# Performance work log

Measured on AMD Instinct MI355X. Metric: run time of the kernel, lower is better.

The kernel has to match this reference:

```python
import jax, jax.numpy as jnp
import numpy as np

B, C, H, W = 4, 3, 256, 256
NCC = 64            # num_conv_channels
N_HIDDEN = 20 - 2   # hidden_block applied num_hiddel_blocks-2 times (shared weights)
EPS = 1e-5          # BatchNorm eps (eval mode: running stats; Dropout2d is identity in eval)


def _bayer_mask():
    # RGGB Bayer pattern: each channel sampled only at its sites, zeros elsewhere
    m = np.zeros((3, H, W), dtype=np.float32)
    m[0, 0::2, 0::2] = 1.0  # R
    m[1, 0::2, 1::2] = 1.0  # G
    m[1, 1::2, 0::2] = 1.0  # G
    m[2, 1::2, 1::2] = 1.0  # B
    return jnp.asarray(m)


def setup_inputs() -> dict:
    key = jax.random.key(0)
    ks = jax.random.split(key, 8)
    X = jax.random.uniform(ks[0], (B, C, H, W), dtype=jnp.float32) * _bayer_mask()[None]
    w_in = jax.random.normal(ks[1], (NCC, 3, 3, 3), dtype=jnp.float32) * 0.15
    b_in = jnp.zeros((NCC,), jnp.float32)
    w_h = jax.random.normal(ks[2], (NCC, NCC, 3, 3), dtype=jnp.float32) * 0.04
    b_h = jnp.zeros((NCC,), jnp.float32)
    w_out = jax.random.normal(ks[3], (3, NCC, 3, 3), dtype=jnp.float32) * 0.04
    b_out = jnp.zeros((3,), jnp.float32)
    def bn_params(n):
        return (jnp.ones((n,), jnp.float32), jnp.zeros((n,), jnp.float32),
                jnp.zeros((n,), jnp.float32), jnp.ones((n,), jnp.float32))
    g_in, be_in, m_in, v_in = bn_params(NCC)
    g_h, be_h, m_h, v_h = bn_params(NCC)
    g_out, be_out, m_out, v_out = bn_params(3)
    return dict(X=X, w_in=w_in, b_in=b_in, g_in=g_in, be_in=be_in, m_in=m_in, v_in=v_in,
                w_h=w_h, b_h=b_h, g_h=g_h, be_h=be_h, m_h=m_h, v_h=v_h,
                w_out=w_out, b_out=b_out, g_out=g_out, be_out=be_out, m_out=m_out, v_out=v_out)


def _conv(x, w, b):
    y = jax.lax.conv_general_dilated(x, w, (1, 1), ((1, 1), (1, 1)),
                                     dimension_numbers=('NCHW', 'OIHW', 'NCHW'))
    return y + b[None, :, None, None]


def _bn(x, g, be, m, v):
    scale = (g / jnp.sqrt(v + EPS))[None, :, None, None]
    return (x - m[None, :, None, None]) * scale + be[None, :, None, None]


def _interpolate_zeros(x):
    # Vectorized masked cross-neighbor average at zero sites, dividing by the
    # count of strictly-positive neighbors (zero-padded borders).
    p = jnp.pad(x, ((0, 0), (0, 0), (1, 1), (1, 1)))
    left = p[:, :, 1:-1, :-2]
    right = p[:, :, 1:-1, 2:]
    top = p[:, :, :-2, 1:-1]
    bottom = p[:, :, 2:, 1:-1]
    nb_sum = left + right + top + bottom
    nb_cnt = ((left > 0).astype(x.dtype) + (right > 0).astype(x.dtype)
              + (top > 0).astype(x.dtype) + (bottom > 0).astype(x.dtype))
    mean = jnp.where(nb_cnt > 0, nb_sum / jnp.maximum(nb_cnt, 1.0), 0.0)
    return jnp.where(x == 0, mean, x)


def reference(X, w_in, b_in, g_in, be_in, m_in, v_in,
              w_h, b_h, g_h, be_h, m_h, v_h,
              w_out, b_out, g_out, be_out, m_out, v_out):
    y = jax.nn.selu(_bn(_conv(X, w_in, b_in), g_in, be_in, m_in, v_in))

    def hidden(y, _):
        y = jax.nn.selu(_bn(_conv(y, w_h, b_h), g_h, be_h, m_h, v_h))
        return y, None

    y, _ = jax.lax.scan(hidden, y, None, length=N_HIDDEN)
    y = jax.nn.selu(_bn(_conv(y, w_out, b_out), g_out, be_out, m_out, v_out))
    return y + _interpolate_zeros(X)
```

## Files before the change

kernel.cpp:

```cpp
#include <hip/hip_runtime.h>

#define EPS 1e-5f
#define SELU_L 1.0507009873554805f
#define SELU_A 1.6732632423543772f
#define SELU_LA (SELU_L * SELU_A)

typedef _Float16 half8 __attribute__((ext_vector_type(8)));
typedef _Float16 half4 __attribute__((ext_vector_type(4)));
typedef float floatx4 __attribute__((ext_vector_type(4)));

__device__ __forceinline__ float selu_f(float x) {
    return x > 0.f ? SELU_L * x : SELU_LA * (__expf(x) - 1.f);
}

__device__ __forceinline__ void gload_lds16(const _Float16* g, _Float16* l) {
    __builtin_amdgcn_global_load_lds(
        (const __attribute__((address_space(1))) void*)g,
        (__attribute__((address_space(3))) void*)l, 16, 0, 0);
}

__global__ __launch_bounds__(256) void k_prep(
    const float* __restrict__ w_h, const float* __restrict__ w_in,
    const float* __restrict__ w_out, _Float16* __restrict__ wb_h,
    _Float16* __restrict__ wb_in, _Float16* __restrict__ wb_out,
    _Float16* __restrict__ zp)
{
    int i = blockIdx.x * 256 + threadIdx.x;
    if (i < 256) zp[i] = (_Float16)0.f;
    if (i < 36864) {
        int t = i >> 11;
        int rem = i & 2047;
        int mi = rem >> 9;
        int L = (rem >> 3) & 63;
        int j = i & 7;
        int co = mi * 16 + (L & 15);
        int ci = ((t & 1) << 5) + ((L >> 4) << 3) + j;
        int s = t >> 1;
        wb_h[i] = (_Float16)w_h[(co * 64 + ci) * 9 + s];
    } else if (i < 36864 + 2048) {
        int e = i - 36864;
        int mi = e >> 9;
        int L = (e >> 3) & 63;
        int j = e & 7;
        int co = mi * 16 + (L & 15);
        int k = ((L >> 4) << 3) + j;
        _Float16 val = (_Float16)0.f;
        if (k < 27) {
            int s = k / 3, ci = k - s * 3;
            val = (_Float16)w_in[(co * 3 + ci) * 9 + s];
        }
        wb_in[e] = val;
    } else if (i < 36864 + 2048 + 9216) {
        int e = i - 36864 - 2048;
        int t = e >> 9;
        int L = (e >> 3) & 63;
        int j = e & 7;
        int co = L & 15;
        int ci = ((t & 1) << 5) + ((L >> 4) << 3) + j;
        int s = t >> 1;
        _Float16 val = (_Float16)0.f;
        if (co < 3) val = (_Float16)w_out[(co * 64 + ci) * 9 + s];
        wb_out[e] = val;
    }
}

__global__ __launch_bounds__(256) void k_conv_in_mfma(
    const float* __restrict__ X, const _Float16* __restrict__ wb,
    const float* __restrict__ bconv, const float* __restrict__ g,
    const float* __restrict__ be, const float* __restrict__ bm,
    const float* __restrict__ bv, _Float16* __restrict__ dst)
{
    __shared__ float s_x[3][18][18];
    __shared__ float s_sc[64], s_bs[64];
    const int tid = threadIdx.x;
    const int w0 = blockIdx.x * 16, h0 = blockIdx.y * 16, b = blockIdx.z;

    if (tid < 64) {
        float sc = g[tid] * rsqrtf(bv[tid] + EPS);
        s_sc[tid] = sc;
        s_bs[tid] = (bconv[tid] - bm[tid]) * sc + be[tid];
    }
    for (int idx = tid; idx < 3 * 324; idx += 256) {
        int ci = idx / 324, rem = idx - ci * 324;
        int r = rem / 18, c = rem - r * 18;
        int gh = h0 - 1 + r, gw = w0 - 1 + c;
        float val = 0.f;
        if ((unsigned)gh < 256u && (unsigned)gw < 256u)
            val = X[((b * 3 + ci) << 16) + (gh << 8) + gw];
        s_x[ci][r][c] = val;
    }
    __syncthreads();

    const int wv = tid >> 6, L = tid & 63, quad = L >> 4, l15 = L & 15;
    half8 a[4];
    #pragma unroll
    for (int mi = 0; mi < 4; ++mi)
        a[mi] = *(const half8*)(wb + (mi * 64 + L) * 8);

    floatx4 acc[4][4];
    #pragma unroll
    for (int mi = 0; mi < 4; ++mi)
        #pragma unroll
        for (int ni = 0; ni < 4; ++ni) acc[mi][ni] = (floatx4){0.f, 0.f, 0.f, 0.f};

    #pragma unroll
    for (int ni = 0; ni < 4; ++ni) {
        half8 bfr;
        #pragma unroll
        for (int j = 0; j < 8; ++j) {
            int k = quad * 8 + j;
            float xv = 0.f;
            if (k < 27) {
                int s = k / 3, ci = k - s * 3;
                int kh = s / 3, kw = s - kh * 3;
                xv = s_x[ci][wv * 4 + ni + kh][l15 + kw];
            }
            bfr[j] = (_Float16)xv;
        }
        #pragma unroll
        for (int mi = 0; mi < 4; ++mi)
            acc[mi][ni] = __builtin_amdgcn_mfma_f32_16x16x32_f16(a[mi], bfr, acc[mi][ni], 0, 0, 0);
    }

    _Float16* db = dst + ((size_t)b << 22);
    #pragma unroll
    for (int mi = 0; mi < 4; ++mi) {
        const int cob = mi * 16 + quad * 4;
        floatx4 sc = *(const floatx4*)(&s_sc[cob]);
        floatx4 bs = *(const floatx4*)(&s_bs[cob]);
        #pragma unroll
        for (int ni = 0; ni < 4; ++ni) {
            half4 ov;
            #pragma unroll
            for (int r = 0; r < 4; ++r)
                ov[r] = (_Float16)selu_f(acc[mi][ni][r] * sc[r] + bs[r]);
            const int row = h0 + wv * 4 + ni, col = w0 + l15;
            *(half4*)(db + ((((row << 8) + col) << 6) + cob)) = ov;
        }
    }
}

__global__ __launch_bounds__(1024) void k_hidden_v13(
    const _Float16* __restrict__ src, const _Float16* __restrict__ wb,
    const float* __restrict__ bconv, const float* __restrict__ g,
    const float* __restrict__ be, const float* __restrict__ bm,
    const float* __restrict__ bv, const _Float16* __restrict__ zp,
    _Float16* __restrict__ dst)
{
    __shared__ _Float16 s_w[36864];
    __shared__ _Float16 s_act[2][20992];
    __shared__ float s_sc[64], s_bs[64];
    const int tid = threadIdx.x;
    const int wv = tid >> 6, L = tid & 63, quad = L >> 4, l15 = L & 15;
    const int rq = wv >> 2, mq = wv & 3;

    if (tid < 64) {
        float sc = g[tid] * rsqrtf(bv[tid] + EPS);
        s_sc[tid] = sc;
        s_bs[tid] = (bconv[tid] - bm[tid]) * sc + be[tid];
    }

    #pragma unroll
    for (int k = 0; k < 5; ++k) {
        const int wc = k * 16 + wv;
        if (wc < 72)
            gload_lds16(wb + ((wc << 6) + L) * 8, &s_w[wc << 9]);
    }

    auto stage = [&](int tau, int buf) {
        const int b = tau >> 8, rem = tau & 255;
        const int h0 = (rem >> 4) << 4, w0 = (rem & 15) << 4;
        const _Float16* sb = src + ((size_t)b << 22);
        #pragma unroll
        for (int k = 0; k < 3; ++k) {
            const int wc = k * 16 + wv;
            if (wc < 41) {
                const int p = (wc << 3) + (L >> 3);
                const int sd = (L & 7) ^ (p & 7);
                const int rp = p / 18, cl = p - rp * 18;
                const int gh = h0 - 1 + rp, gw = w0 - 1 + cl;
                const _Float16* gp = (p < 324 && (unsigned)gh < 256u && (unsigned)gw < 256u)
                    ? sb + ((((gh << 8) + gw) << 6) + (sd << 3)) : zp;
                gload_lds16(gp, &s_act[buf][wc << 9]);
            }
        }
    };

    const int tau0 = blockIdx.x << 2;
    stage(tau0, 0);
    __syncthreads();

    for (int ti = 0; ti < 4; ++ti) {
        const int tau = tau0 + ti, cur = ti & 1;
        if (ti < 3) stage(tau + 1, cur ^ 1);

        floatx4 acc[4];
        #pragma unroll
        for (int ni = 0; ni < 4; ++ni) acc[ni] = (floatx4){0.f, 0.f, 0.f, 0.f};

        const _Float16* bufp = &s_act[cur][0];
        #pragma unroll
        for (int h = 0; h < 2; ++h) {
            const int sb8 = (h << 2) + quad;
            #pragma unroll
            for (int kw = 0; kw < 3; ++kw) {
                half8 ac[3];
                #pragma unroll
                for (int kh = 0; kh < 3; ++kh) {
                    const int t = ((kh * 3 + kw) << 1) + h;
                    ac[kh] = *(const half8*)(&s_w[((t * 4 + mq) * 64 + L) * 8]);
                }
                #pragma unroll
                for (int j = 0; j < 6; ++j) {
                    const int p = (rq * 4 + j) * 18 + l15 + kw;
                    half8 bfr = *(const half8*)(bufp + (p << 6) + (((p & 7) ^ sb8) << 3));
                    #pragma unroll
                    for (int kh = 0; kh < 3; ++kh) {
                        const int ni = j - kh;
                        if (ni >= 0 && ni < 4)
                            acc[ni] = __builtin_amdgcn_mfma_f32_16x16x32_f16(ac[kh], bfr, acc[ni], 0, 0, 0);
                    }
                }
            }
        }

        const int b = tau >> 8, rem = tau & 255;
        const int h0 = (rem >> 4) << 4, w0 = (rem & 15) << 4;
        _Float16* db = dst + ((size_t)b << 22);
        const int cob = mq * 16 + quad * 4;
        floatx4 sc = *(const floatx4*)(&s_sc[cob]);
        floatx4 bs = *(const floatx4*)(&s_bs[cob]);
        #pragma unroll
        for (int ni = 0; ni < 4; ++ni) {
            half4 ov;
            #pragma unroll
            for (int r = 0; r < 4; ++r)
                ov[r] = (_Float16)selu_f(acc[ni][r] * sc[r] + bs[r]);
            const int row = h0 + rq * 4 + ni, col = w0 + l15;
            *(half4*)(db + ((((row << 8) + col) << 6) + cob)) = ov;
        }
        __syncthreads();
    }
}

__global__ __launch_bounds__(256) void k_conv_out_mfma(
    const _Float16* __restrict__ src, const _Float16* __restrict__ wb,
    const float* __restrict__ bconv, const float* __restrict__ g,
    const float* __restrict__ be, const float* __restrict__ bm,
    const float* __restrict__ bv, const float* __restrict__ X,
    float* __restrict__ out)
{
    __shared__ _Float16 s_in[324 * 72];
    const int tid = threadIdx.x;
    const int w0 = blockIdx.x * 16, h0 = blockIdx.y * 16, b = blockIdx.z;
    const _Float16* sb = src + ((size_t)b << 22);

    for (int idx = tid; idx < 2592; idx += 256) {
        int r = idx / 144, cpos = idx - r * 144;
        int col = cpos >> 3, sub = cpos & 7;
        int gh = h0 - 1 + r, gw = w0 - 1 + col;
        half8 val = {0, 0, 0, 0, 0, 0, 0, 0};
        if ((unsigned)gh < 256u && (unsigned)gw < 256u)
            val = *(const half8*)(sb + ((((gh << 8) + gw) << 6) + (sub << 3)));
        *(half8*)(&s_in[(r * 18 + col) * 72 + (sub << 3)]) = val;
    }
    __syncthreads();

    const int wv = tid >> 6, L = tid & 63, quad = L >> 4, l15 = L & 15;
    floatx4 acc[4];
    #pragma unroll
    for (int ni = 0; ni < 4; ++ni) acc[ni] = (floatx4){0.f, 0.f, 0.f, 0.f};

    #pragma unroll
    for (int t = 0; t < 18; ++t) {
        const int s = t >> 1, ci0 = (t & 1) << 5;
        const int kh = s / 3, kw = s - kh * 3;
        half8 a = *(const half8*)(wb + (t * 64 + L) * 8);
        #pragma unroll
        for (int ni = 0; ni < 4; ++ni) {
            const int row = wv * 4 + ni + kh, col = l15 + kw;
            half8 bfr = *(const half8*)(&s_in[(row * 18 + col) * 72 + ci0 + quad * 8]);
            acc[ni] = __builtin_amdgcn_mfma_f32_16x16x32_f16(a, bfr, acc[ni], 0, 0, 0);
        }
    }

    if (quad == 0) {
        float sc[3], bs[3];
        #pragma unroll
        for (int co = 0; co < 3; ++co) {
            sc[co] = g[co] * rsqrtf(bv[co] + EPS);
            bs[co] = (bconv[co] - bm[co]) * sc[co] + be[co];
        }
        #pragma unroll
        for (int ni = 0; ni < 4; ++ni) {
            const int h = h0 + wv * 4 + ni, wc = w0 + l15;
            #pragma unroll
            for (int co = 0; co < 3; ++co) {
                float val = selu_f(acc[ni][co] * sc[co] + bs[co]);
                const float* Xc = X + ((size_t)(b * 3 + co) << 16);
                float x = Xc[(h << 8) + wc];
                float res;
                if (x == 0.f) {
                    float lft = (wc > 0)   ? Xc[(h << 8) + wc - 1] : 0.f;
                    float rgt = (wc < 255) ? Xc[(h << 8) + wc + 1] : 0.f;
                    float top = (h > 0)    ? Xc[((h - 1) << 8) + wc] : 0.f;
                    float bot = (h < 255)  ? Xc[((h + 1) << 8) + wc] : 0.f;
                    float sm = lft + rgt + top + bot;
                    int cnt = (lft > 0.f) + (rgt > 0.f) + (top > 0.f) + (bot > 0.f);
                    res = cnt > 0 ? sm / (float)cnt : 0.f;
                } else {
                    res = x;
                }
                out[((b * 3 + co) << 16) + (h << 8) + wc] = val + res;
            }
        }
    }
}

extern "C" void kernel_launch(void* const* d_in, const int* in_sizes, int n_in,
                              void* d_out, int out_size, void* d_ws, size_t ws_size,
                              hipStream_t stream) {
    (void)in_sizes; (void)n_in; (void)out_size; (void)ws_size;
    const float* X    = (const float*)d_in[0];
    const float* w_in = (const float*)d_in[1];
    const float* b_in = (const float*)d_in[2];
    const float* g_in = (const float*)d_in[3];
    const float* be_in= (const float*)d_in[4];
    const float* m_in = (const float*)d_in[5];
    const float* v_in = (const float*)d_in[6];
    const float* w_h  = (const float*)d_in[7];
    const float* b_h  = (const float*)d_in[8];
    const float* g_h  = (const float*)d_in[9];
    const float* be_h = (const float*)d_in[10];
    const float* m_h  = (const float*)d_in[11];
    const float* v_h  = (const float*)d_in[12];
    const float* w_o  = (const float*)d_in[13];
    const float* b_o  = (const float*)d_in[14];
    const float* g_o  = (const float*)d_in[15];
    const float* be_o = (const float*)d_in[16];
    const float* m_o  = (const float*)d_in[17];
    const float* v_o  = (const float*)d_in[18];
    float* out = (float*)d_out;

    _Float16* act0  = (_Float16*)d_ws;
    _Float16* act1  = act0 + ((size_t)1 << 24);
    _Float16* wb_h  = act1 + ((size_t)1 << 24);
    _Float16* wb_in = wb_h + 36864;
    _Float16* wb_out= wb_in + 2048;
    _Float16* zp    = wb_out + 9216;

    dim3 grid(16, 16, 4), block(256);
    k_prep<<<188, 256, 0, stream>>>(w_h, w_in, w_o, wb_h, wb_in, wb_out, zp);
    k_conv_in_mfma<<<grid, block, 0, stream>>>(X, wb_in, b_in, g_in, be_in, m_in, v_in, act0);
    _Float16* src = act0;
    _Float16* dst = act1;
    for (int i = 0; i < 18; ++i) {
        k_hidden_v13<<<256, 1024, 0, stream>>>(src, wb_h, b_h, g_h, be_h, m_h, v_h, zp, dst);
        _Float16* t = src; src = dst; dst = t;
    }
    k_conv_out_mfma<<<grid, block, 0, stream>>>(src, wb_out, b_o, g_o, be_o, m_o, v_o, X, out);
}
```

Baseline: 597.9 us.

## Fuse eighteen hidden-layer launches into one persistent kernel with grid barrier

Replaces the 18 per-layer launches of the hidden conv kernel with a single persistent kernel. It loops over layers, ping-pongs between the two activation buffers, and separates layers with a software grid barrier (an atomic counter zeroed in the prep kernel). This is meant to remove per-launch overhead and the repeated reload of the weights into LDS. In exchange it adds barrier spin latency, relies on all 256 blocks being co-resident, and relies on cross-XCD cache coherence of activations written by other blocks.

```diff
diff --git a/kernel.cpp b/kernel.cpp
--- a/kernel.cpp
+++ b/kernel.cpp
@@ -23,9 +23,10 @@
     const float* __restrict__ w_h, const float* __restrict__ w_in,
     const float* __restrict__ w_out, _Float16* __restrict__ wb_h,
     _Float16* __restrict__ wb_in, _Float16* __restrict__ wb_out,
-    _Float16* __restrict__ zp)
+    _Float16* __restrict__ zp, unsigned* __restrict__ bar)
 {
     int i = blockIdx.x * 256 + threadIdx.x;
+    if (i == 0) *bar = 0u;
     if (i < 256) zp[i] = (_Float16)0.f;
     if (i < 36864) {
         int t = i >> 11;
@@ -140,12 +141,13 @@
     }
 }
 
-__global__ __launch_bounds__(1024) void k_hidden_v13(
-    const _Float16* __restrict__ src, const _Float16* __restrict__ wb,
+__global__ __launch_bounds__(1024) void k_hidden_all(
+    _Float16* __restrict__ act0, _Float16* __restrict__ act1,
+    const _Float16* __restrict__ wb,
     const float* __restrict__ bconv, const float* __restrict__ g,
     const float* __restrict__ be, const float* __restrict__ bm,
     const float* __restrict__ bv, const _Float16* __restrict__ zp,
-    _Float16* __restrict__ dst)
+    unsigned* __restrict__ bar)
 {
     __shared__ _Float16 s_w[36864];
     __shared__ _Float16 s_act[2][20992];
@@ -167,10 +169,10 @@
             gload_lds16(wb + ((wc << 6) + L) * 8, &s_w[wc << 9]);
     }
 
-    auto stage = [&](int tau, int buf) {
+    auto stage = [&](const _Float16* sp, int tau, int buf) {
         const int b = tau >> 8, rem = tau & 255;
         const int h0 = (rem >> 4) << 4, w0 = (rem & 15) << 4;
-        const _Float16* sb = src + ((size_t)b << 22);
+        const _Float16* sb = sp + ((size_t)b << 22);
         #pragma unroll
         for (int k = 0; k < 3; ++k) {
             const int wc = k * 16 + wv;
@@ -187,59 +189,80 @@
     };
 
     const int tau0 = blockIdx.x << 2;
-    stage(tau0, 0);
+    _Float16* src = act0;
+    _Float16* dst = act1;
+
+    stage(src, tau0, 0);
     __syncthreads();
 
-    for (int ti = 0; ti < 4; ++ti) {
-        const int tau = tau0 + ti, cur = ti & 1;
-        if (ti < 3) stage(tau + 1, cur ^ 1);
-
-        floatx4 acc[4];
-        #pragma unroll
-        for (int ni = 0; ni < 4; ++ni) acc[ni] = (floatx4){0.f, 0.f, 0.f, 0.f};
-
-        const _Float16* bufp = &s_act[cur][0];
-        #pragma unroll
-        for (int h = 0; h < 2; ++h) {
-            const int sb8 = (h << 2) + quad;
-            #pragma unroll
-            for (int kw = 0; kw < 3; ++kw) {
-                half8 ac[3];
+    for (int layer = 0; layer < 18; ++layer) {
+        for (int ti = 0; ti < 4; ++ti) {
+            const int tau = tau0 + ti, cur = ti & 1;
+            if (ti < 3) stage(src, tau + 1, cur ^ 1);
+
+            floatx4 acc[4];
+            #pragma unroll
+            for (int ni = 0; ni < 4; ++ni) acc[ni] = (floatx4){0.f, 0.f, 0.f, 0.f};
+
+            const _Float16* bufp = &s_act[cur][0];
+            #pragma unroll
+            for (int h = 0; h < 2; ++h) {
+                const int sb8 = (h << 2) + quad;
                 #pragma unroll
-                for (int kh = 0; kh < 3; ++kh) {
-                    const int t = ((kh * 3 + kw) << 1) + h;
-                    ac[kh] = *(const half8*)(&s_w[((t * 4 + mq) * 64 + L) * 8]);
-                }
-                #pragma unroll
-                for (int j = 0; j < 6; ++j) {
-                    const int p = (rq * 4 + j) * 18 + l15 + kw;
-                    half8 bfr = *(const half8*)(bufp + (p << 6) + (((p & 7) ^ sb8) << 3));
+                for (int kw = 0; kw < 3; ++kw) {
+                    half8 ac[3];
                     #pragma unroll
                     for (int kh = 0; kh < 3; ++kh) {
-                        const int ni = j - kh;
-                        if (ni >= 0 && ni < 4)
-                            acc[ni] = __builtin_amdgcn_mfma_f32_16x16x32_f16(ac[kh], bfr, acc[ni], 0, 0, 0);
+                        const int t = ((kh * 3 + kw) << 1) + h;
+                        ac[kh] = *(const half8*)(&s_w[((t * 4 + mq) * 64 + L) * 8]);
+                    }
+                    #pragma unroll
+                    for (int j = 0; j < 6; ++j) {
+                        const int p = (rq * 4 + j) * 18 + l15 + kw;
+                        half8 bfr = *(const half8*)(bufp + (p << 6) + (((p & 7) ^ sb8) << 3));
+                        #pragma unroll
+                        for (int kh = 0; kh < 3; ++kh) {
+                            const int ni = j - kh;
+                            if (ni >= 0 && ni < 4)
+                                acc[ni] = __builtin_amdgcn_mfma_f32_16x16x32_f16(ac[kh], bfr, acc[ni], 0, 0, 0);
+                        }
                     }
                 }
             }
-        }
-
-        const int b = tau >> 8, rem = tau & 255;
-        const int h0 = (rem >> 4) << 4, w0 = (rem & 15) << 4;
-        _Float16* db = dst + ((size_t)b << 22);
-        const int cob = mq * 16 + quad * 4;
-        floatx4 sc = *(const floatx4*)(&s_sc[cob]);
-        floatx4 bs = *(const floatx4*)(&s_bs[cob]);
-        #pragma unroll
-        for (int ni = 0; ni < 4; ++ni) {
-            half4 ov;
-            #pragma unroll
-            for (int r = 0; r < 4; ++r)
-                ov[r] = (_Float16)selu_f(acc[ni][r] * sc[r] + bs[r]);
-            const int row = h0 + rq * 4 + ni, col = w0 + l15;
-            *(half4*)(db + ((((row << 8) + col) << 6) + cob)) = ov;
-        }
-        __syncthreads();
+
+            const int b = tau >> 8, rem = tau & 255;
+            const int h0 = (rem >> 4) << 4, w0 = (rem & 15) << 4;
+            _Float16* db = dst + ((size_t)b << 22);
+            const int cob = mq * 16 + quad * 4;
+            floatx4 sc = *(const floatx4*)(&s_sc[cob]);
+            floatx4 bs = *(const floatx4*)(&s_bs[cob]);
+            #pragma unroll
+            for (int ni = 0; ni < 4; ++ni) {
+                half4 ov;
+                #pragma unroll
+                for (int r = 0; r < 4; ++r)
+                    ov[r] = (_Float16)selu_f(acc[ni][r] * sc[r] + bs[r]);
+                const int row = h0 + rq * 4 + ni, col = w0 + l15;
+                *(half4*)(db + ((((row << 8) + col) << 6) + cob)) = ov;
+            }
+            __syncthreads();
+        }
+
+        if (layer < 17) {
+            if (tid == 0) {
+                __threadfence();
+                atomicAdd(bar, 1u);
+                const unsigned tgt = 256u * (unsigned)(layer + 1);
+                while (atomicAdd(bar, 0u) < tgt)
+                    __builtin_amdgcn_s_sleep(32);
+                __threadfence();
+            }
+            __syncthreads();
+
+            _Float16* t = src; src = dst; dst = t;
+            stage(src, tau0, 0);
+            __syncthreads();
+        }
     }
 }
 
@@ -348,15 +371,11 @@
     _Float16* wb_in = wb_h + 36864;
     _Float16* wb_out= wb_in + 2048;
     _Float16* zp    = wb_out + 9216;
+    unsigned* bar   = (unsigned*)(zp + 256);
 
     dim3 grid(16, 16, 4), block(256);
-    k_prep<<<188, 256, 0, stream>>>(w_h, w_in, w_o, wb_h, wb_in, wb_out, zp);
+    k_prep<<<188, 256, 0, stream>>>(w_h, w_in, w_o, wb_h, wb_in, wb_out, zp, bar);
     k_conv_in_mfma<<<grid, block, 0, stream>>>(X, wb_in, b_in, g_in, be_in, m_in, v_in, act0);
-    _Float16* src = act0;
-    _Float16* dst = act1;
-    for (int i = 0; i < 18; ++i) {
-        k_hidden_v13<<<256, 1024, 0, stream>>>(src, wb_h, b_h, g_h, be_h, m_h, v_h, zp, dst);
-        _Float16* t = src; src = dst; dst = t;
-    }
-    k_conv_out_mfma<<<grid, block, 0, stream>>>(src, wb_out, b_o, g_o, be_o, m_o, v_o, X, out);
-}
+    k_hidden_all<<<256, 1024, 0, stream>>>(act0, act1, wb_h, b_h, g_h, be_h, m_h, v_h, zp, bar);
+    k_conv_out_mfma<<<grid, block, 0, stream>>>(act0, wb_out, b_o, g_o, be_o, m_o, v_o, X, out);
+}
```

Result: slower. 1.001 ms (+67.5%).
